# Kernel optimization log

Measured on AMD Instinct MI355X. Metric: run time of the kernel, lower is better.

Reference implementation:

```python
import jax, jax.numpy as jnp
import numpy as np

N = 20000      # nodes
E = 320000     # directed edges (before self-loops)
IN, HID, HEADS, OUT = 512, 256, 4, 256
NEG_SLOPE = 0.2  # PyG GATConv default


def setup_inputs() -> dict:
    key = jax.random.key(0)
    ks = jax.random.split(key, 10)
    x = jax.random.normal(ks[0], (N, IN), jnp.float32)
    edge_index = jax.random.randint(ks[1], (2, E), 0, N, jnp.int32)
    W1 = jax.random.normal(ks[2], (IN, HEADS * HID), jnp.float32) / np.sqrt(IN).astype(np.float32)
    att_src1 = jax.random.normal(ks[3], (HEADS, HID), jnp.float32) * 0.1
    att_dst1 = jax.random.normal(ks[4], (HEADS, HID), jnp.float32) * 0.1
    b1 = jnp.zeros((HEADS * HID,), jnp.float32)
    W2 = jax.random.normal(ks[5], (HEADS * HID, OUT), jnp.float32) / np.sqrt(HEADS * HID).astype(np.float32)
    att_src2 = jax.random.normal(ks[6], (1, OUT), jnp.float32) * 0.1
    att_dst2 = jax.random.normal(ks[7], (1, OUT), jnp.float32) * 0.1
    b2 = jnp.zeros((OUT,), jnp.float32)
    return {"x": x, "edge_index": edge_index, "W1": W1, "att_src1": att_src1,
            "att_dst1": att_dst1, "b1": b1, "W2": W2, "att_src2": att_src2,
            "att_dst2": att_dst2, "b2": b2}


def _segment_softmax(logits, seg, num_segments):
    # softmax over edges grouped by destination node (per head)
    m = jax.ops.segment_max(logits, seg, num_segments=num_segments)
    ex = jnp.exp(logits - m[seg])
    s = jax.ops.segment_sum(ex, seg, num_segments=num_segments)
    return ex / (s[seg] + 1e-16)


def _gat_conv(x, src, dst, W, att_src, att_dst, bias, heads, ch, num_nodes, concat):
    # PyG GATConv: h = W x (per head); alpha_e = softmax_dst(LeakyReLU(a_s.h_src + a_d.h_dst))
    h = (x @ W).reshape(num_nodes, heads, ch)          # [N,H,C]
    a_s = (h * att_src).sum(-1)                        # [N,H]
    a_d = (h * att_dst).sum(-1)                        # [N,H]
    logits = jax.nn.leaky_relu(a_s[src] + a_d[dst], NEG_SLOPE)   # [E,H]
    alpha = _segment_softmax(logits, dst, num_nodes)             # [E,H]
    msg = h[src] * alpha[:, :, None]                             # [E,H,C]
    out = jax.ops.segment_sum(msg, dst, num_segments=num_nodes)  # [N,H,C]
    out = out.reshape(num_nodes, heads * ch) if concat else out.mean(axis=1)
    return out + bias


def reference(x, edge_index, W1, att_src1, att_dst1, b1, W2, att_src2, att_dst2, b2):
    # add self-loops (PyG default add_self_loops=True)
    loop = jnp.arange(N, dtype=edge_index.dtype)
    src = jnp.concatenate([edge_index[0], loop])
    dst = jnp.concatenate([edge_index[1], loop])
    h = jax.nn.elu(_gat_conv(x, src, dst, W1, att_src1, att_dst1, b1, HEADS, HID, N, True))
    return _gat_conv(h, src, dst, W2, att_src2, att_dst2, b2, 1, OUT, N, False)
```

## Files before the change

### kernel.cpp

```cpp
#include <hip/hip_runtime.h>
#include <hip/hip_bf16.h>
#include <cfloat>
#include <math.h>

#define N_NODES 20000
#define M_PAD   20096
#define N_EDGES 320000
#define TOT_E   (N_EDGES + N_NODES)
#define EPAD    512
#define PS      (TOT_E + EPAD)
#define IN_F    512
#define HID     256
#define HEADS   4
#define OUT_F   256
#define H1DIM   (HEADS * HID)
#define NEG_SLOPE 0.2f

typedef __attribute__((ext_vector_type(8))) __bf16 bf16x8;
typedef __attribute__((ext_vector_type(4))) __bf16 bf16x4;
typedef __attribute__((ext_vector_type(4))) float f32x4;

__device__ __forceinline__ float lrelu(float x) { return x >= 0.f ? x : NEG_SLOPE * x; }
__device__ __forceinline__ float elu_lite(float x) { return x > 0.f ? x : __expf(x) - 1.f; }

__global__ void k_count(const int* __restrict__ ei, int* __restrict__ deg) {
  int e = blockIdx.x * 256 + threadIdx.x;
  if (e >= TOT_E) return;
  int dst = (e < N_EDGES) ? ei[N_EDGES + e] : (e - N_EDGES);
  atomicAdd(&deg[dst], 1);
}

__global__ void k_scan(const int* __restrict__ deg, int* __restrict__ off) {
  __shared__ int part[256];
  int tid = threadIdx.x;
  const int chunk = (N_NODES + 255) / 256;
  int s0 = tid * chunk;
  int s1 = s0 + chunk; if (s1 > N_NODES) s1 = N_NODES; if (s0 > N_NODES) s0 = N_NODES;
  int s = 0;
  for (int i = s0; i < s1; ++i) s += deg[i];
  part[tid] = s;
  __syncthreads();
  for (int d = 1; d < 256; d <<= 1) {
    int v = (tid >= d) ? part[tid - d] : 0;
    __syncthreads();
    part[tid] += v;
    __syncthreads();
  }
  int run = (tid == 0) ? 0 : part[tid - 1];
  for (int i = s0; i < s1; ++i) { off[i] = run; run += deg[i]; }
  if (tid == 255) off[N_NODES] = run;
}

__global__ void k_fill(const int* __restrict__ ei, const int* __restrict__ off,
                       int* __restrict__ cur, int* __restrict__ csr_src) {
  int e = blockIdx.x * 256 + threadIdx.x;
  if (e >= TOT_E) return;
  int src, dst;
  if (e < N_EDGES) { src = ei[e]; dst = ei[N_EDGES + e]; }
  else             { src = dst = e - N_EDGES; }
  int pos = atomicAdd(&cur[dst], 1);
  csr_src[off[dst] + pos] = src;
}

__global__ void k_f2b(const float* __restrict__ in, __bf16* __restrict__ out, int n4) {
  int i = blockIdx.x * 256 + threadIdx.x;
  if (i >= n4) return;
  float4 v = ((const float4*)in)[i];
  bf16x4 o = { (__bf16)v.x, (__bf16)v.y, (__bf16)v.z, (__bf16)v.w };
  ((bf16x4*)out)[i] = o;
}

__global__ void k_tr_f2b(const float* __restrict__ in, __bf16* __restrict__ out,
                         int R, int Cc) {
  __shared__ float tile[32][33];
  int c0 = blockIdx.x * 32, r0 = blockIdx.y * 32;
  int tx = threadIdx.x & 31, ty = threadIdx.x >> 5;
  for (int rr = ty; rr < 32; rr += 8)
    tile[rr][tx] = in[(size_t)(r0 + rr) * Cc + c0 + tx];
  __syncthreads();
  for (int rr = ty; rr < 32; rr += 8)
    out[(size_t)(c0 + rr) * R + r0 + tx] = (__bf16)tile[tx][rr];
}

__global__ __launch_bounds__(256) void k_gemm_bf16(
    const __bf16* __restrict__ A,
    const __bf16* __restrict__ Bt,
    __bf16* __restrict__ Cb,
    const float* __restrict__ attS, const float* __restrict__ attD,
    float* __restrict__ asO, float* __restrict__ adO, int hstride,
    int M, int N, int K)
{
  __shared__ char lds[32768];
  char* As = lds;
  char* Bs = lds + 16384;

  const int t = threadIdx.x;
  const int lane = t & 63;
  const int wid = t >> 6;
  const int wm = wid >> 1, wn = wid & 1;
  const int row0 = blockIdx.y * 128;
  const int col0 = blockIdx.x * 128;

  f32x4 acc[4][4];
#pragma unroll
  for (int i = 0; i < 4; ++i)
#pragma unroll
    for (int j = 0; j < 4; ++j) acc[i][j] = (f32x4){0.f, 0.f, 0.f, 0.f};

  for (int k0 = 0; k0 < K; k0 += 64) {
#pragma unroll
    for (int i = 0; i < 4; ++i) {
      int j = i * 256 + t;
      int r = j >> 3;
      int cc = (j & 7) ^ (r & 7);
      const __bf16* gp = A + (size_t)(row0 + r) * K + k0 + cc * 8;
      __builtin_amdgcn_global_load_lds(
          (const __attribute__((address_space(1))) void*)gp,
          (__attribute__((address_space(3))) void*)(As + j * 16), 16, 0, 0);
    }
#pragma unroll
    for (int i = 0; i < 4; ++i) {
      int j = i * 256 + t;
      int r = j >> 3;
      int cc = (j & 7) ^ (r & 7);
      const __bf16* gp = Bt + (size_t)(col0 + r) * K + k0 + cc * 8;
      __builtin_amdgcn_global_load_lds(
          (const __attribute__((address_space(1))) void*)gp,
          (__attribute__((address_space(3))) void*)(Bs + j * 16), 16, 0, 0);
    }
    __syncthreads();

#pragma unroll
    for (int ks = 0; ks < 2; ++ks) {
      bf16x8 af[4], bfr[4];
#pragma unroll
      for (int i = 0; i < 4; ++i) {
        int rA = wm * 64 + i * 16 + (lane & 15);
        int chA = (ks * 4 + (lane >> 4)) ^ (rA & 7);
        af[i] = *(const bf16x8*)(As + rA * 128 + chA * 16);
        int rB = wn * 64 + i * 16 + (lane & 15);
        int chB = (ks * 4 + (lane >> 4)) ^ (rB & 7);
        bfr[i] = *(const bf16x8*)(Bs + rB * 128 + chB * 16);
      }
#pragma unroll
      for (int i = 0; i < 4; ++i)
#pragma unroll
        for (int jn = 0; jn < 4; ++jn)
          acc[i][jn] = __builtin_amdgcn_mfma_f32_16x16x32_bf16(
              af[i], bfr[jn], acc[i][jn], 0, 0, 0);
    }
    __syncthreads();
  }

#pragma unroll
  for (int i = 0; i < 4; ++i) {
    int growb = row0 + wm * 64 + i * 16 + (lane >> 4) * 4;
#pragma unroll
    for (int jn = 0; jn < 4; ++jn) {
      int gcol = col0 + wn * 64 + jn * 16 + (lane & 15);
#pragma unroll
      for (int r = 0; r < 4; ++r) {
        int grow = growb + r;
        if (grow < M) Cb[(size_t)grow * N + gcol] = (__bf16)acc[i][jn][r];
      }
    }
  }

  int head = (col0 + wn * 64) >> 8;
  float sv[4], dv[4];
#pragma unroll
  for (int jn = 0; jn < 4; ++jn) {
    int c = col0 + wn * 64 + jn * 16 + (lane & 15);
    sv[jn] = attS[c];
    dv[jn] = attD[c];
  }
#pragma unroll
  for (int i = 0; i < 4; ++i) {
#pragma unroll
    for (int r = 0; r < 4; ++r) {
      float pa = 0.f, pd = 0.f;
#pragma unroll
      for (int jn = 0; jn < 4; ++jn) {
        pa = fmaf(acc[i][jn][r], sv[jn], pa);
        pd = fmaf(acc[i][jn][r], dv[jn], pd);
      }
#pragma unroll
      for (int d = 1; d < 16; d <<= 1) {
        pa += __shfl_xor(pa, d);
        pd += __shfl_xor(pd, d);
      }
      if ((lane & 15) == 0) {
        int grow = row0 + wm * 64 + i * 16 + (lane >> 4) * 4 + r;
        if (grow < M) {
          atomicAdd(&asO[(size_t)grow * hstride + head], pa);
          atomicAdd(&adO[(size_t)grow * hstride + head], pd);
        }
      }
    }
  }
}

__global__ void k_w1(const int* __restrict__ off, const int* __restrict__ csr,
                     const float* __restrict__ as, const float* __restrict__ ad,
                     float* __restrict__ wnP, float* __restrict__ inv) {
  int n = blockIdx.x;
  int lane = threadIdx.x;
  int beg = off[n], end = off[n + 1];
  float4 adv = *(const float4*)&ad[n * 4];
  float p0 = 0.f, p1 = 0.f, p2 = 0.f, p3 = 0.f;
  for (int p = beg + lane; p < end; p += 64) {
    int s = csr[p];
    float4 av = *(const float4*)&as[s * 4];
    float w0 = __expf(lrelu(av.x + adv.x));
    float w1 = __expf(lrelu(av.y + adv.y));
    float w2 = __expf(lrelu(av.z + adv.z));
    float w3 = __expf(lrelu(av.w + adv.w));
    p0 += w0; p1 += w1; p2 += w2; p3 += w3;
    wnP[p] = w0;
    wnP[PS + p] = w1;
    wnP[2 * PS + p] = w2;
    wnP[3 * PS + p] = w3;
  }
#pragma unroll
  for (int d = 32; d; d >>= 1) {
    p0 += __shfl_xor(p0, d); p1 += __shfl_xor(p1, d);
    p2 += __shfl_xor(p2, d); p3 += __shfl_xor(p3, d);
  }
  if (lane == 0) {
    float4 iv = {1.f / (p0 + 1e-16f), 1.f / (p1 + 1e-16f),
                 1.f / (p2 + 1e-16f), 1.f / (p3 + 1e-16f)};
    *(float4*)&inv[n * 4] = iv;
  }
}

__global__ void k_w2(const int* __restrict__ off, const int* __restrict__ csr,
                     const float* __restrict__ as, const float* __restrict__ ad,
                     float* __restrict__ wn, float* __restrict__ inv) {
  int n = blockIdx.x;
  int lane = threadIdx.x;
  int beg = off[n], end = off[n + 1];
  float adv = ad[n];
  float ps = 0.f;
  for (int p = beg + lane; p < end; p += 64) {
    int s = csr[p];
    float w = __expf(lrelu(as[s] + adv));
    wn[p] = w;
    ps += w;
  }
#pragma unroll
  for (int d = 32; d; d >>= 1) ps += __shfl_xor(ps, d);
  if (lane == 0) inv[n] = 1.f / (ps + 1e-16f);
}

__global__ __launch_bounds__(256) void k_gather1(
    const int* __restrict__ off, const int* __restrict__ csr,
    const __bf16* __restrict__ h1b, const float* __restrict__ wnP,
    const float* __restrict__ inv, const float* __restrict__ b1,
    __bf16* __restrict__ heluB) {
  int bid = blockIdx.x;
  int slice = bid & 7;
  int head = slice >> 1;
  int cb = slice * 128;
  int w = threadIdx.x >> 6, lane = threadIdx.x & 63;
  int sub = lane >> 4;
  int cg = lane & 15;
  int n = (bid >> 3) * 4 + w;
  int beg = off[n], end = off[n + 1];
  int deg = end - beg;
  int it = (deg + 3) >> 2;

  float acc[8] = {0.f, 0.f, 0.f, 0.f, 0.f, 0.f, 0.f, 0.f};
  const __bf16* hb = h1b + cb + cg * 8;
  const float* wp = wnP + (size_t)head * PS;
#pragma unroll 2
  for (int i = 0; i < it; ++i) {
    int e = beg + i * 4 + sub;
    bool v = (e < end);
    int s = v ? csr[e] : 0;
    float wv = v ? wp[e] : 0.f;
    uint4 u = *(const uint4*)(hb + (size_t)s * H1DIM);
    acc[0] = fmaf(wv, __uint_as_float(u.x << 16), acc[0]);
    acc[1] = fmaf(wv, __uint_as_float(u.x & 0xffff0000u), acc[1]);
    acc[2] = fmaf(wv, __uint_as_float(u.y << 16), acc[2]);
    acc[3] = fmaf(wv, __uint_as_float(u.y & 0xffff0000u), acc[3]);
    acc[4] = fmaf(wv, __uint_as_float(u.z << 16), acc[4]);
    acc[5] = fmaf(wv, __uint_as_float(u.z & 0xffff0000u), acc[5]);
    acc[6] = fmaf(wv, __uint_as_float(u.w << 16), acc[6]);
    acc[7] = fmaf(wv, __uint_as_float(u.w & 0xffff0000u), acc[7]);
  }
#pragma unroll
  for (int k = 0; k < 8; ++k) {
    acc[k] += __shfl_xor(acc[k], 16);
    acc[k] += __shfl_xor(acc[k], 32);
  }
  if (sub == 0) {
    float iv = inv[n * 4 + head];
    float4 bv0 = *(const float4*)(b1 + cb + cg * 8);
    float4 bv1 = *(const float4*)(b1 + cb + cg * 8 + 4);
    float bb[8] = {bv0.x, bv0.y, bv0.z, bv0.w, bv1.x, bv1.y, bv1.z, bv1.w};
    bf16x8 o;
#pragma unroll
    for (int k = 0; k < 8; ++k) {
      float v = acc[k] * iv + bb[k];
      o[k] = (__bf16)elu_lite(v);
    }
    *(bf16x8*)(heluB + (size_t)n * H1DIM + cb + cg * 8) = o;
  }
}

__global__ __launch_bounds__(256) void k_gather2(
    const int* __restrict__ off, const int* __restrict__ csr,
    const __bf16* __restrict__ h2b, const float* __restrict__ wn,
    const float* __restrict__ inv, const float* __restrict__ b2,
    float* __restrict__ out) {
  int bid = blockIdx.x;
  int slice = bid & 3;
  int cb = slice * 64;
  int w = threadIdx.x >> 6, lane = threadIdx.x & 63;
  int sub = lane >> 3;
  int cg = lane & 7;
  int n = (bid >> 2) * 4 + w;
  int beg = off[n], end = off[n + 1];
  int deg = end - beg;
  int it = (deg + 7) >> 3;

  float acc[8] = {0.f, 0.f, 0.f, 0.f, 0.f, 0.f, 0.f, 0.f};
  const __bf16* hb = h2b + cb + cg * 8;
#pragma unroll 2
  for (int i = 0; i < it; ++i) {
    int e = beg + i * 8 + sub;
    bool v = (e < end);
    int s = v ? csr[e] : 0;
    float wv = v ? wn[e] : 0.f;
    uint4 u = *(const uint4*)(hb + (size_t)s * OUT_F);
    acc[0] = fmaf(wv, __uint_as_float(u.x << 16), acc[0]);
    acc[1] = fmaf(wv, __uint_as_float(u.x & 0xffff0000u), acc[1]);
    acc[2] = fmaf(wv, __uint_as_float(u.y << 16), acc[2]);
    acc[3] = fmaf(wv, __uint_as_float(u.y & 0xffff0000u), acc[3]);
    acc[4] = fmaf(wv, __uint_as_float(u.z << 16), acc[4]);
    acc[5] = fmaf(wv, __uint_as_float(u.z & 0xffff0000u), acc[5]);
    acc[6] = fmaf(wv, __uint_as_float(u.w << 16), acc[6]);
    acc[7] = fmaf(wv, __uint_as_float(u.w & 0xffff0000u), acc[7]);
  }
#pragma unroll
  for (int k = 0; k < 8; ++k) {
    acc[k] += __shfl_xor(acc[k], 8);
    acc[k] += __shfl_xor(acc[k], 16);
    acc[k] += __shfl_xor(acc[k], 32);
  }
  if (sub == 0) {
    float iv = inv[n];
    float4 bv0 = *(const float4*)(b2 + cb + cg * 8);
    float4 bv1 = *(const float4*)(b2 + cb + cg * 8 + 4);
    float* op = out + (size_t)n * OUT_F + cb + cg * 8;
    float4 o0 = {acc[0] * iv + bv0.x, acc[1] * iv + bv0.y,
                 acc[2] * iv + bv0.z, acc[3] * iv + bv0.w};
    float4 o1 = {acc[4] * iv + bv1.x, acc[5] * iv + bv1.y,
                 acc[6] * iv + bv1.z, acc[7] * iv + bv1.w};
    *(float4*)op = o0;
    *(float4*)(op + 4) = o1;
  }
}

extern "C" void kernel_launch(void* const* d_in, const int* in_sizes, int n_in,
                              void* d_out, int out_size, void* d_ws, size_t ws_size,
                              hipStream_t stream) {
  const float* x      = (const float*)d_in[0];
  const int*   ei     = (const int*)d_in[1];
  const float* W1     = (const float*)d_in[2];
  const float* att_s1 = (const float*)d_in[3];
  const float* att_d1 = (const float*)d_in[4];
  const float* b1     = (const float*)d_in[5];
  const float* W2     = (const float*)d_in[6];
  const float* att_s2 = (const float*)d_in[7];
  const float* att_d2 = (const float*)d_in[8];
  const float* b2     = (const float*)d_in[9];
  float* out = (float*)d_out;

  char* w = (char*)d_ws;
  auto alloc = [&](size_t bytes) {
    char* p = w;
    w += (bytes + 255) & ~(size_t)255;
    return p;
  };
  int*    deg   = (int*)alloc((size_t)N_NODES * 4);
  int*    off   = (int*)alloc((size_t)(N_NODES + 1) * 4);
  int*    cur   = (int*)alloc((size_t)N_NODES * 4);
  int*    csr   = (int*)alloc((size_t)PS * 4);
  float*  as1   = (float*)alloc((size_t)N_NODES * HEADS * 4);
  float*  ad1   = (float*)alloc((size_t)N_NODES * HEADS * 4);
  float*  as2   = (float*)alloc((size_t)N_NODES * 4);
  float*  ad2   = (float*)alloc((size_t)N_NODES * 4);
  float*  wnP   = (float*)alloc((size_t)PS * HEADS * 4);
  float*  inv1  = (float*)alloc((size_t)N_NODES * HEADS * 4);
  float*  wn2   = (float*)alloc((size_t)PS * 4);
  float*  inv2  = (float*)alloc((size_t)N_NODES * 4);
  __bf16* xb    = (__bf16*)alloc((size_t)M_PAD * IN_F * 2);
  __bf16* w1t   = (__bf16*)alloc((size_t)H1DIM * IN_F * 2);
  __bf16* w2t   = (__bf16*)alloc((size_t)OUT_F * H1DIM * 2);
  __bf16* h1b   = (__bf16*)alloc((size_t)M_PAD * H1DIM * 2);
  __bf16* heluB = (__bf16*)alloc((size_t)M_PAD * H1DIM * 2);
  __bf16* h2b   = (__bf16*)alloc((size_t)M_PAD * OUT_F * 2);
  if ((size_t)(w - (char*)d_ws) > ws_size) return;

  hipMemsetAsync(deg, 0, (size_t)N_NODES * 4, stream);
  hipMemsetAsync(cur, 0, (size_t)N_NODES * 4, stream);
  hipMemsetAsync(csr + TOT_E, 0, (size_t)EPAD * 4, stream);
  hipMemsetAsync(as1, 0, (size_t)N_NODES * HEADS * 4, stream);
  hipMemsetAsync(ad1, 0, (size_t)N_NODES * HEADS * 4, stream);
  hipMemsetAsync(as2, 0, (size_t)N_NODES * 4, stream);
  hipMemsetAsync(ad2, 0, (size_t)N_NODES * 4, stream);

  k_count<<<(TOT_E + 255) / 256, 256, 0, stream>>>(ei, deg);
  k_scan<<<1, 256, 0, stream>>>(deg, off);
  k_fill<<<(TOT_E + 255) / 256, 256, 0, stream>>>(ei, off, cur, csr);

  int n4 = N_NODES * IN_F / 4;
  k_f2b<<<(n4 + 255) / 256, 256, 0, stream>>>(x, xb, n4);
  k_tr_f2b<<<dim3(H1DIM / 32, IN_F / 32), 256, 0, stream>>>(W1, w1t, IN_F, H1DIM);
  k_tr_f2b<<<dim3(OUT_F / 32, H1DIM / 32), 256, 0, stream>>>(W2, w2t, H1DIM, OUT_F);

  k_gemm_bf16<<<dim3(H1DIM / 128, M_PAD / 128), 256, 0, stream>>>(
      xb, w1t, h1b, att_s1, att_d1, as1, ad1, HEADS, N_NODES, H1DIM, IN_F);
  k_w1<<<N_NODES, 64, 0, stream>>>(off, csr, as1, ad1, wnP, inv1);
  k_gather1<<<(N_NODES / 4) * 8, 256, 0, stream>>>(off, csr, h1b, wnP, inv1, b1, heluB);

  k_gemm_bf16<<<dim3(OUT_F / 128, M_PAD / 128), 256, 0, stream>>>(
      heluB, w2t, h2b, att_s2, att_d2, as2, ad2, 1, N_NODES, OUT_F, H1DIM);
  k_w2<<<N_NODES, 64, 0, stream>>>(off, csr, as2, ad2, wn2, inv2);
  k_gather2<<<(N_NODES / 4) * 4, 256, 0, stream>>>(off, csr, h2b, wn2, inv2, b2, out);
}
```

Measured before the change: 342.5 us.

## Map each lane group to its own node in gather kernels, dropping shuffle reductions

The gather kernels now give each 16-lane (layer 1) or 8-lane (layer 2) subgroup its own destination node, instead of having the whole wavefront share one node and split its edges across subgroups. This removes the cross-lane shuffle reduction and the single-subgroup store at the end, and shrinks the grid by 4x and 8x. Each subgroup walks its node's edges sequentially up to the wave's maximum degree, so degree imbalance within a wave leaves lanes idle. Loads of csr and weights become per-node sequential and less coalesced.

```diff
diff --git a/kernel.cpp b/kernel.cpp
--- a/kernel.cpp
+++ b/kernel.cpp
@@ -262,20 +262,22 @@
   int head = slice >> 1;
   int cb = slice * 128;
   int w = threadIdx.x >> 6, lane = threadIdx.x & 63;
-  int sub = lane >> 4;
+  int g = lane >> 4;
   int cg = lane & 15;
-  int n = (bid >> 3) * 4 + w;
+  int n = (bid >> 3) * 16 + w * 4 + g;
   int beg = off[n], end = off[n + 1];
   int deg = end - beg;
-  int it = (deg + 3) >> 2;
+  int itmax = deg;
+  itmax = max(itmax, __shfl_xor(itmax, 16));
+  itmax = max(itmax, __shfl_xor(itmax, 32));
 
   float acc[8] = {0.f, 0.f, 0.f, 0.f, 0.f, 0.f, 0.f, 0.f};
   const __bf16* hb = h1b + cb + cg * 8;
   const float* wp = wnP + (size_t)head * PS;
 #pragma unroll 2
-  for (int i = 0; i < it; ++i) {
-    int e = beg + i * 4 + sub;
-    bool v = (e < end);
+  for (int i = 0; i < itmax; ++i) {
+    int e = beg + i;
+    bool v = (i < deg);
     int s = v ? csr[e] : 0;
     float wv = v ? wp[e] : 0.f;
     uint4 u = *(const uint4*)(hb + (size_t)s * H1DIM);
@@ -288,24 +290,18 @@
     acc[6] = fmaf(wv, __uint_as_float(u.w << 16), acc[6]);
     acc[7] = fmaf(wv, __uint_as_float(u.w & 0xffff0000u), acc[7]);
   }
+
+  float iv = inv[n * 4 + head];
+  float4 bv0 = *(const float4*)(b1 + cb + cg * 8);
+  float4 bv1 = *(const float4*)(b1 + cb + cg * 8 + 4);
+  float bb[8] = {bv0.x, bv0.y, bv0.z, bv0.w, bv1.x, bv1.y, bv1.z, bv1.w};
+  bf16x8 o;
 #pragma unroll
   for (int k = 0; k < 8; ++k) {
-    acc[k] += __shfl_xor(acc[k], 16);
-    acc[k] += __shfl_xor(acc[k], 32);
-  }
-  if (sub == 0) {
-    float iv = inv[n * 4 + head];
-    float4 bv0 = *(const float4*)(b1 + cb + cg * 8);
-    float4 bv1 = *(const float4*)(b1 + cb + cg * 8 + 4);
-    float bb[8] = {bv0.x, bv0.y, bv0.z, bv0.w, bv1.x, bv1.y, bv1.z, bv1.w};
-    bf16x8 o;
-#pragma unroll
-    for (int k = 0; k < 8; ++k) {
-      float v = acc[k] * iv + bb[k];
-      o[k] = (__bf16)elu_lite(v);
-    }
-    *(bf16x8*)(heluB + (size_t)n * H1DIM + cb + cg * 8) = o;
-  }
+    float v = acc[k] * iv + bb[k];
+    o[k] = (__bf16)elu_lite(v);
+  }
+  *(bf16x8*)(heluB + (size_t)n * H1DIM + cb + cg * 8) = o;
 }
 
 __global__ __launch_bounds__(256) void k_gather2(
@@ -317,19 +313,22 @@
   int slice = bid & 3;
   int cb = slice * 64;
   int w = threadIdx.x >> 6, lane = threadIdx.x & 63;
-  int sub = lane >> 3;
+  int g = lane >> 3;
   int cg = lane & 7;
-  int n = (bid >> 2) * 4 + w;
+  int n = (bid >> 2) * 32 + w * 8 + g;
   int beg = off[n], end = off[n + 1];
   int deg = end - beg;
-  int it = (deg + 7) >> 3;
+  int itmax = deg;
+  itmax = max(itmax, __shfl_xor(itmax, 8));
+  itmax = max(itmax, __shfl_xor(itmax, 16));
+  itmax = max(itmax, __shfl_xor(itmax, 32));
 
   float acc[8] = {0.f, 0.f, 0.f, 0.f, 0.f, 0.f, 0.f, 0.f};
   const __bf16* hb = h2b + cb + cg * 8;
 #pragma unroll 2
-  for (int i = 0; i < it; ++i) {
-    int e = beg + i * 8 + sub;
-    bool v = (e < end);
+  for (int i = 0; i < itmax; ++i) {
+    int e = beg + i;
+    bool v = (i < deg);
     int s = v ? csr[e] : 0;
     float wv = v ? wn[e] : 0.f;
     uint4 u = *(const uint4*)(hb + (size_t)s * OUT_F);
@@ -342,24 +341,17 @@
     acc[6] = fmaf(wv, __uint_as_float(u.w << 16), acc[6]);
     acc[7] = fmaf(wv, __uint_as_float(u.w & 0xffff0000u), acc[7]);
   }
-#pragma unroll
-  for (int k = 0; k < 8; ++k) {
-    acc[k] += __shfl_xor(acc[k], 8);
-    acc[k] += __shfl_xor(acc[k], 16);
-    acc[k] += __shfl_xor(acc[k], 32);
-  }
-  if (sub == 0) {
-    float iv = inv[n];
-    float4 bv0 = *(const float4*)(b2 + cb + cg * 8);
-    float4 bv1 = *(const float4*)(b2 + cb + cg * 8 + 4);
-    float* op = out + (size_t)n * OUT_F + cb + cg * 8;
-    float4 o0 = {acc[0] * iv + bv0.x, acc[1] * iv + bv0.y,
-                 acc[2] * iv + bv0.z, acc[3] * iv + bv0.w};
-    float4 o1 = {acc[4] * iv + bv1.x, acc[5] * iv + bv1.y,
-                 acc[6] * iv + bv1.z, acc[7] * iv + bv1.w};
-    *(float4*)op = o0;
-    *(float4*)(op + 4) = o1;
-  }
+
+  float iv = inv[n];
+  float4 bv0 = *(const float4*)(b2 + cb + cg * 8);
+  float4 bv1 = *(const float4*)(b2 + cb + cg * 8 + 4);
+  float* op = out + (size_t)n * OUT_F + cb + cg * 8;
+  float4 o0 = {acc[0] * iv + bv0.x, acc[1] * iv + bv0.y,
+               acc[2] * iv + bv0.z, acc[3] * iv + bv0.w};
+  float4 o1 = {acc[4] * iv + bv1.x, acc[5] * iv + bv1.y,
+               acc[6] * iv + bv1.z, acc[7] * iv + bv1.w};
+  *(float4*)op = o0;
+  *(float4*)(op + 4) = o1;
 }
 
 extern "C" void kernel_launch(void* const* d_in, const int* in_sizes, int n_in,
@@ -423,10 +415,10 @@
   k_gemm_bf16<<<dim3(H1DIM / 128, M_PAD / 128), 256, 0, stream>>>(
       xb, w1t, h1b, att_s1, att_d1, as1, ad1, HEADS, N_NODES, H1DIM, IN_F);
   k_w1<<<N_NODES, 64, 0, stream>>>(off, csr, as1, ad1, wnP, inv1);
-  k_gather1<<<(N_NODES / 4) * 8, 256, 0, stream>>>(off, csr, h1b, wnP, inv1, b1, heluB);
+  k_gather1<<<(N_NODES / 16) * 8, 256, 0, stream>>>(off, csr, h1b, wnP, inv1, b1, heluB);
 
   k_gemm_bf16<<<dim3(OUT_F / 128, M_PAD / 128), 256, 0, stream>>>(
       heluB, w2t, h2b, att_s2, att_d2, as2, ad2, 1, N_NODES, OUT_F, H1DIM);
   k_w2<<<N_NODES, 64, 0, stream>>>(off, csr, as2, ad2, wn2, inv2);
-  k_gather2<<<(N_NODES / 4) * 4, 256, 0, stream>>>(off, csr, h2b, wn2, inv2, b2, out);
-}
+  k_gather2<<<(N_NODES / 32) * 4, 256, 0, stream>>>(off, csr, h2b, wn2, inv2, b2, out);
+}
```

After: 328.6 us. -4.1%, faster.
